# Optimization experiments

Hardware: AMD Instinct MI355X
Metric: run time of the kernel (lower is better)

Reference implementation:

```python
import jax, jax.numpy as jnp
import numpy as np

WEIGHT = 1.0
_EPS = 0.008856          # (6/29)^3 threshold used by skimage rgb2lab
_KAPPA = 7.787           # 1/3 * (29/6)^2 scaled form used by skimage
# sRGB -> XYZ (D65) luminance (Y) row of the conversion matrix, as in skimage
_YR, _YG, _YB = 0.2126729, 0.7151522, 0.0721750


def _luminance_L(rgb):
    """rgb: (B,3,H,W) in [-1,1] -> L channel of CIE Lab, shape (B,H,W)."""
    s = (rgb + 1.0) * 0.5                                   # to [0,1]
    # inverse sRGB companding (gamma expansion)
    lin = jnp.where(s > 0.04045, ((s + 0.055) / 1.055) ** 2.4, s / 12.92)
    Y = _YR * lin[:, 0] + _YG * lin[:, 1] + _YB * lin[:, 2]  # (B,H,W), Yn=1
    # f(Y): cube root above threshold, linear segment below (safe-where for grads)
    Y_safe = jnp.where(Y > _EPS, Y, 1.0)
    f = jnp.where(Y > _EPS, jnp.cbrt(Y_safe), _KAPPA * Y + 16.0 / 116.0)
    return 116.0 * f - 16.0                                  # L in [0,100]


def setup_inputs() -> dict:
    key = jax.random.key(0)
    k1, k2 = jax.random.split(key)
    shape = (64, 3, 512, 512)
    generated = jax.random.uniform(k1, shape, dtype=jnp.float32, minval=-1.0, maxval=1.0)
    target = jax.random.uniform(k2, shape, dtype=jnp.float32, minval=-1.0, maxval=1.0)
    return {"generated": generated, "target": target}


def reference(generated, target):
    L_gen = _luminance_L(generated)
    L_tgt = _luminance_L(target)
    loss = jnp.mean(jnp.abs(L_gen - L_tgt))  # F.l1_loss
    return WEIGHT * loss
```

## Files before the change

### kernel.cpp

```cpp
#include <hip/hip_runtime.h>


#define HW4       65536
#define CHW4      196608
#define NPIX      16777216
#define NGRP      4194304
#define NTH       524288

__device__ __forceinline__ float fast_log2(float x) {
#if __has_builtin(__builtin_amdgcn_logf)
    return __builtin_amdgcn_logf(x);
#else
    return __log2f(x);
#endif
}
__device__ __forceinline__ float fast_exp2(float x) {
#if __has_builtin(__builtin_amdgcn_exp2f)
    return __builtin_amdgcn_exp2f(x);
#else
    return exp2f(x);
#endif
}

__device__ __forceinline__ float srgb_expand(float x) {
    float a  = fmaf(x, 0.47393364f, 0.52606636f);
    float hi = fast_exp2(2.4f * fast_log2(a));
    float lo = fmaf(x, 0.03869969f, 0.03869969f);
    return (x > -0.9191f) ? hi : lo;
}

__device__ __forceinline__ float lab_f(float r, float g, float b) {
    float lr = srgb_expand(r);
    float lg = srgb_expand(g);
    float lb = srgb_expand(b);
    float Y  = fmaf(0.2126729f, lr, fmaf(0.7151522f, lg, 0.0721750f * lb));
    float cb = fast_exp2(0.333333333333f * fast_log2(Y));
    float lin = fmaf(7.787f, Y, 16.0f / 116.0f);
    return (Y > 0.008856f) ? cb : lin;
}

__device__ __forceinline__ float group_absdiff(
        float4 gr, float4 gg, float4 gb,
        float4 tr, float4 tg, float4 tb) {
    float s;
    s  = fabsf(lab_f(gr.x, gg.x, gb.x) - lab_f(tr.x, tg.x, tb.x));
    s += fabsf(lab_f(gr.y, gg.y, gb.y) - lab_f(tr.y, tg.y, tb.y));
    s += fabsf(lab_f(gr.z, gg.z, gb.z) - lab_f(tr.z, tg.z, tb.z));
    s += fabsf(lab_f(gr.w, gg.w, gb.w) - lab_f(tr.w, tg.w, tb.w));
    return s;
}

__global__ void zero_out_kernel(float* out) {
    if (threadIdx.x == 0) out[0] = 0.0f;
}

__global__ __launch_bounds__(256, 4) void lum_loss_kernel(
        const float* __restrict__ gen,
        const float* __restrict__ tgt,
        float* __restrict__ out) {
    const float4* gp = (const float4*)gen;
    const float4* tp = (const float4*)tgt;

    int tid = blockIdx.x * 256 + threadIdx.x;

    float acc[4] = {0.0f, 0.0f, 0.0f, 0.0f};

    #pragma unroll
    for (int j = 0; j < 8; ++j) {
        int grp  = tid + j * NTH;
        int b    = grp >> 16;
        int i    = grp & 65535;
        int base = b * CHW4 + i;

        float4 gr = gp[base];
        float4 gg = gp[base + HW4];
        float4 gb = gp[base + 2 * HW4];
        float4 tr = tp[base];
        float4 tg = tp[base + HW4];
        float4 tb = tp[base + 2 * HW4];

        acc[j & 3] += group_absdiff(gr, gg, gb, tr, tg, tb);
    }

    float a = ((acc[0] + acc[1]) + (acc[2] + acc[3])) * 116.0f;

    #pragma unroll
    for (int off = 32; off > 0; off >>= 1)
        a += __shfl_down(a, off, 64);

    __shared__ float smem[4];
    int lane = threadIdx.x & 63;
    int wave = threadIdx.x >> 6;
    if (lane == 0) smem[wave] = a;
    __syncthreads();

    if (threadIdx.x == 0) {
        float s = smem[0] + smem[1] + smem[2] + smem[3];
        atomicAdd(out, s * (1.0f / (float)NPIX));
    }
}

extern "C" void kernel_launch(void* const* d_in, const int* in_sizes, int n_in,
                              void* d_out, int out_size, void* d_ws, size_t ws_size,
                              hipStream_t stream) {
    const float* gen = (const float*)d_in[0];
    const float* tgt = (const float*)d_in[1];
    float* out = (float*)d_out;

    zero_out_kernel<<<1, 64, 0, stream>>>(out);
    lum_loss_kernel<<<2048, 256, 0, stream>>>(gen, tgt, out);
}
```

Before: 391.5 us.

## Use one-shot threads with two adjacent groups each and larger grid

Replaces the 8-iteration strided loop per thread with a single pass where each thread loads two adjacent float4 groups per channel for both inputs. Block size goes to 512 and the grid to 4096 blocks, so far more threads are in flight and all loads are issued up front. This is meant to raise memory-level parallelism and achieved bandwidth. The cost is more per-thread index setup relative to work and twice as many atomic additions.

```diff
diff --git a/kernel.cpp b/kernel.cpp
--- a/kernel.cpp
+++ b/kernel.cpp
@@ -1,11 +1,9 @@
 #include <hip/hip_runtime.h>
 
 
-#define HW4       65536
-#define CHW4      196608
-#define NPIX      16777216
-#define NGRP      4194304
-#define NTH       524288
+#define HW4   65536
+#define CHW4  196608
+#define NPIX  16777216
 
 __device__ __forceinline__ float fast_log2(float x) {
 #if __has_builtin(__builtin_amdgcn_logf)
@@ -54,48 +52,49 @@
     if (threadIdx.x == 0) out[0] = 0.0f;
 }
 
-__global__ __launch_bounds__(256, 4) void lum_loss_kernel(
+__global__ __launch_bounds__(512, 4) void lum_loss_kernel(
         const float* __restrict__ gen,
         const float* __restrict__ tgt,
         float* __restrict__ out) {
     const float4* gp = (const float4*)gen;
     const float4* tp = (const float4*)tgt;
 
-    int tid = blockIdx.x * 256 + threadIdx.x;
+    int t    = blockIdx.x * 512 + threadIdx.x;
+    int g0   = t << 1;
+    int b    = g0 >> 16;
+    int i    = g0 & 65535;
+    int base = b * CHW4 + i;
 
-    float acc[4] = {0.0f, 0.0f, 0.0f, 0.0f};
+    float4 gr0 = gp[base];
+    float4 gr1 = gp[base + 1];
+    float4 gg0 = gp[base + HW4];
+    float4 gg1 = gp[base + HW4 + 1];
+    float4 gb0 = gp[base + 2 * HW4];
+    float4 gb1 = gp[base + 2 * HW4 + 1];
+    float4 tr0 = tp[base];
+    float4 tr1 = tp[base + 1];
+    float4 tg0 = tp[base + HW4];
+    float4 tg1 = tp[base + HW4 + 1];
+    float4 tb0 = tp[base + 2 * HW4];
+    float4 tb1 = tp[base + 2 * HW4 + 1];
 
-    #pragma unroll
-    for (int j = 0; j < 8; ++j) {
-        int grp  = tid + j * NTH;
-        int b    = grp >> 16;
-        int i    = grp & 65535;
-        int base = b * CHW4 + i;
-
-        float4 gr = gp[base];
-        float4 gg = gp[base + HW4];
-        float4 gb = gp[base + 2 * HW4];
-        float4 tr = tp[base];
-        float4 tg = tp[base + HW4];
-        float4 tb = tp[base + 2 * HW4];
-
-        acc[j & 3] += group_absdiff(gr, gg, gb, tr, tg, tb);
-    }
-
-    float a = ((acc[0] + acc[1]) + (acc[2] + acc[3])) * 116.0f;
+    float a = group_absdiff(gr0, gg0, gb0, tr0, tg0, tb0)
+            + group_absdiff(gr1, gg1, gb1, tr1, tg1, tb1);
+    a *= 116.0f;
 
     #pragma unroll
     for (int off = 32; off > 0; off >>= 1)
         a += __shfl_down(a, off, 64);
 
-    __shared__ float smem[4];
+    __shared__ float smem[8];
     int lane = threadIdx.x & 63;
     int wave = threadIdx.x >> 6;
     if (lane == 0) smem[wave] = a;
     __syncthreads();
 
     if (threadIdx.x == 0) {
-        float s = smem[0] + smem[1] + smem[2] + smem[3];
+        float s = ((smem[0] + smem[1]) + (smem[2] + smem[3]))
+                + ((smem[4] + smem[5]) + (smem[6] + smem[7]));
         atomicAdd(out, s * (1.0f / (float)NPIX));
     }
 }
@@ -108,5 +107,5 @@
     float* out = (float*)d_out;
 
     zero_out_kernel<<<1, 64, 0, stream>>>(out);
-    lum_loss_kernel<<<2048, 256, 0, stream>>>(gen, tgt, out);
+    lum_loss_kernel<<<4096, 512, 0, stream>>>(gen, tgt, out);
 }
```

Result: no change. 386.7 us (-1.2%).
